# Kernel optimization log

Measured on AMD Instinct MI355X. Metric: run time of the kernel, lower is better.

Reference implementation:

```python
import jax, jax.numpy as jnp
import numpy as np

VOCAB = 100000
SHORTLIST = 10000  # cutoffs = [10000, 20000, 40000, 80000], n_clusters = 4
B, T, D = 1024, 128, 1024


def setup_inputs() -> dict:
    key = jax.random.key(0)
    ks = jax.random.split(key, 12)
    s = 0.02  # realistic init scale for weights
    inp = {
        "features": jax.random.normal(ks[0], (B, D), jnp.float32),
        "head_weight": jax.random.normal(ks[1], (SHORTLIST + 4, D), jnp.float32) * s,
        "proj0": jax.random.normal(ks[2], (512, D), jnp.float32) * s,
        "out0": jax.random.normal(ks[3], (10000, 512), jnp.float32) * s,
        "proj1": jax.random.normal(ks[4], (256, D), jnp.float32) * s,
        "out1": jax.random.normal(ks[5], (20000, 256), jnp.float32) * s,
        "proj2": jax.random.normal(ks[6], (128, D), jnp.float32) * s,
        "out2": jax.random.normal(ks[7], (40000, 128), jnp.float32) * s,
        "proj3": jax.random.normal(ks[8], (64, D), jnp.float32) * s,
        "out3": jax.random.normal(ks[9], (20000, 64), jnp.float32) * s,
        "discard_probs": jax.random.uniform(ks[10], (VOCAB,), jnp.float32),
        "targets": jax.random.randint(ks[11], (B, T), 0, VOCAB, jnp.int64),
        "target_mask": jnp.ones((B, T), jnp.bool_),
    }
    return inp


def _adaptive_log_prob(x, head_weight, projs, outs):
    # head: shortlist logits + one logit per tail cluster
    head_lp = jax.nn.log_softmax(x @ head_weight.T, axis=-1)  # [B, SHORTLIST+4]
    parts = [head_lp[:, :SHORTLIST]]
    for i, (pw, ow) in enumerate(zip(projs, outs)):
        cluster_logits = (x @ pw.T) @ ow.T  # [B, osz]
        parts.append(jax.nn.log_softmax(cluster_logits, axis=-1)
                     + head_lp[:, SHORTLIST + i:SHORTLIST + i + 1])
    return jnp.concatenate(parts, axis=-1)  # [B, VOCAB]


def reference(features, head_weight, proj0, out0, proj1, out1, proj2, out2,
              proj3, out3, discard_probs, targets, target_mask):
    # dropout is identity in eval/reference mode
    logprob = _adaptive_log_prob(features, head_weight,
                                 (proj0, proj1, proj2, proj3),
                                 (out0, out1, out2, out3))
    lp_t = jnp.take_along_axis(logprob, targets, axis=1)        # [B, T]
    w = (1.0 - discard_probs[targets]) * target_mask.astype(lp_t.dtype)
    per_sample = jnp.sum(-lp_t * w, axis=1) / jnp.sum(w, axis=1)  # [B]
    return jnp.sum(per_sample) / (targets.shape[0] + 1e-5)
```

## Files before the change

### kernel.cpp

```cpp
#include <hip/hip_runtime.h>
#include <cstdint>


typedef unsigned short u16;
typedef __attribute__((ext_vector_type(4))) float f32x4;
typedef __attribute__((ext_vector_type(8))) __bf16 bf16x8;
typedef __attribute__((ext_vector_type(4))) unsigned int u32x4;

__device__ __forceinline__ u16 f2bf(float f){
  unsigned u = __float_as_uint(f);
  u += 0x7FFFu + ((u >> 16) & 1u);
  return (u16)(u >> 16);
}

__device__ __forceinline__ float wave_sum(float v){
  #pragma unroll
  for (int d = 1; d < 64; d <<= 1) v += __shfl_xor(v, d, 64);
  return v;
}

__device__ __forceinline__ float wave_dot_l(const u16* a_lds, const u16* b, int len, int lane){
  float s = 0.f;
  for (int k = lane*8; k < len; k += 512){
    u32x4 va = *(const u32x4*)(a_lds + k);
    u32x4 vb = *(const u32x4*)(b + k);
    #pragma unroll
    for (int i = 0; i < 4; i++){
      unsigned ua = va[i], ub = vb[i];
      s = fmaf(__uint_as_float(ua << 16),        __uint_as_float(ub << 16),        s);
      s = fmaf(__uint_as_float(ua & 0xFFFF0000u), __uint_as_float(ub & 0xFFFF0000u), s);
    }
  }
  return wave_sum(s);
}

struct CvtSeg { const float* src; u16* dst; unsigned start; };
struct CvtTab { CvtSeg s[10]; unsigned total; };

__global__ __launch_bounds__(256) void cvt_bf16(CvtTab t){
  unsigned stride = gridDim.x * blockDim.x;
  for (unsigned c = blockIdx.x*blockDim.x + threadIdx.x; c < t.total; c += stride){
    int si = 0;
    #pragma unroll
    for (int i = 1; i < 10; i++) if (c >= t.s[i].start) si = i;
    unsigned lo = c - t.s[si].start;
    const float4* sp = (const float4*)t.s[si].src + (size_t)lo*2;
    float4 f0 = sp[0], f1 = sp[1];
    uint4 d;
    d.x = (unsigned)f2bf(f0.x) | ((unsigned)f2bf(f0.y) << 16);
    d.y = (unsigned)f2bf(f0.z) | ((unsigned)f2bf(f0.w) << 16);
    d.z = (unsigned)f2bf(f1.x) | ((unsigned)f2bf(f1.y) << 16);
    d.w = (unsigned)f2bf(f1.z) | ((unsigned)f2bf(f1.w) << 16);
    ((uint4*)t.s[si].dst)[lo] = d;
  }
}

struct GSeg { const u16* A; const u16* B; float* part; u16* C; float* gates;
              int lda, N, K, ntiles, tileStart, ldc; };
struct GTab { GSeg seg[5]; int nseg; };

__global__ __launch_bounds__(256, 3) void gemm_all(GTab tab){
  __shared__ u16 ldsA[128*64];
  __shared__ u16 ldsB[128*64];
  __shared__ float msLds[128][2];

  int by = blockIdx.y;
  int s = 0;
  #pragma unroll
  for (int i = 1; i < 5; i++)
    if (i < tab.nseg && by >= tab.seg[i].tileStart) s = i;
  const u16* Ab = tab.seg[s].A;
  const u16* Bb = tab.seg[s].B;
  float* part   = tab.seg[s].part;
  u16* Cc       = tab.seg[s].C;
  float* gatesp = tab.seg[s].gates;
  int lda = tab.seg[s].lda, N = tab.seg[s].N, K = tab.seg[s].K;
  int ntiles = tab.seg[s].ntiles, ldc = tab.seg[s].ldc;
  int tileN = by - tab.seg[s].tileStart;
  int n0 = tileN * 128;
  int row0 = blockIdx.x * 128;

  int tid = threadIdx.x;
  int wid = tid >> 6, lane = tid & 63;
  int wr = wid >> 1, wc = wid & 1;
  int qr = lane >> 4, ln = lane & 15;

  const char* baseA = (const char*)(Ab + (size_t)row0*lda);
  const char* baseB = (const char*)Bb;
  unsigned offA[4], offB[4];
  #pragma unroll
  for (int t = 0; t < 4; t++){
    int c = t*256 + tid, row = c >> 3, jj = (c & 7) ^ (row & 7);
    offA[t] = (unsigned)(row*lda + jj*8) * 2u;
    int nr = n0 + row; if (nr >= N) nr = N - 1;
    offB[t] = (unsigned)(nr*K + jj*8) * 2u;
  }

  u32x4 pa[4], pb[4];
  #pragma unroll
  for (int t = 0; t < 4; t++){ pa[t] = *(const u32x4*)(baseA + offA[t]);
                               pb[t] = *(const u32x4*)(baseB + offB[t]); }

  f32x4 acc[4][4];
  const f32x4 zero = {0.f, 0.f, 0.f, 0.f};
  #pragma unroll
  for (int i = 0; i < 4; i++)
    #pragma unroll
    for (int j = 0; j < 4; j++) acc[i][j] = zero;

  int nkt = K >> 6;
  for (int kt = 0; kt < nkt; kt++){
    __syncthreads();
    #pragma unroll
    for (int t = 0; t < 4; t++){
      *(u32x4*)((char*)ldsA + (size_t)(t*256 + tid)*16) = pa[t];
      *(u32x4*)((char*)ldsB + (size_t)(t*256 + tid)*16) = pb[t];
    }
    __syncthreads();
    if (kt + 1 < nkt){
      unsigned kb = (unsigned)(kt + 1) * 128u;
      #pragma unroll
      for (int t = 0; t < 4; t++){ pa[t] = *(const u32x4*)(baseA + offA[t] + kb);
                                   pb[t] = *(const u32x4*)(baseB + offB[t] + kb); }
    }
    #pragma unroll
    for (int ks = 0; ks < 2; ks++){
      bf16x8 av[4], bv[4];
      #pragma unroll
      for (int mt = 0; mt < 4; mt++){
        int rl = wr*64 + mt*16 + ln;
        int ch = rl*8 + ((ks*4 + qr) ^ (rl & 7));
        av[mt] = *(const bf16x8*)((const char*)ldsA + ch*16);
      }
      #pragma unroll
      for (int nt = 0; nt < 4; nt++){
        int rl = wc*64 + nt*16 + ln;
        int ch = rl*8 + ((ks*4 + qr) ^ (rl & 7));
        bv[nt] = *(const bf16x8*)((const char*)ldsB + ch*16);
      }
      #pragma unroll
      for (int mt = 0; mt < 4; mt++)
        #pragma unroll
        for (int nt = 0; nt < 4; nt++)
          acc[mt][nt] = __builtin_amdgcn_mfma_f32_16x16x32_bf16(av[mt], bv[nt], acc[mt][nt], 0, 0, 0);
    }
  }

  if (part){
    #pragma unroll
    for (int mt = 0; mt < 4; mt++){
      #pragma unroll
      for (int r = 0; r < 4; r++){
        float ss = 0.f;
        #pragma unroll
        for (int nt = 0; nt < 4; nt++){
          int col = n0 + wc*64 + nt*16 + ln;
          if (col < N){
            float v = acc[mt][nt][r];
            ss += __expf(v);
            if (gatesp && col >= 10000){
              int row = row0 + wr*64 + mt*16 + qr*4 + r;
              gatesp[row*4 + (col - 10000)] = v;
            }
          }
        }
        ss += __shfl_xor(ss, 1, 64);
        ss += __shfl_xor(ss, 2, 64);
        ss += __shfl_xor(ss, 4, 64);
        ss += __shfl_xor(ss, 8, 64);
        if (ln == 0) msLds[wr*64 + mt*16 + qr*4 + r][wc] = ss;
      }
    }
    __syncthreads();
    if (tid < 128)
      part[(size_t)(row0 + tid)*ntiles + tileN] = msLds[tid][0] + msLds[tid][1];
  } else {
    #pragma unroll
    for (int mt = 0; mt < 4; mt++)
      #pragma unroll
      for (int nt = 0; nt < 4; nt++)
        #pragma unroll
        for (int r = 0; r < 4; r++){
          int col = n0 + wc*64 + nt*16 + ln;
          if (col < N){
            int row = row0 + wr*64 + mt*16 + qr*4 + r;
            Cc[(size_t)row*ldc + col] = f2bf(acc[mt][nt][r]);
          }
        }
  }
}

struct LseTab { const float* base[5]; int ntiles[5]; float* lse; };

__global__ __launch_bounds__(256) void lse_reduce(LseTab t){
  int widx = blockIdx.x*4 + (threadIdx.x >> 6);
  int lane = threadIdx.x & 63;
  int mat = widx >> 10, row = widx & 1023;
  const float* p = t.base[mat] + (size_t)row * t.ntiles[mat];
  float s = 0.f;
  for (int i = lane; i < t.ntiles[mat]; i += 64) s += p[i];
  s = wave_sum(s);
  if (lane == 0) t.lse[mat*1024 + row] = __logf(s);
}

struct GatherArgs {
  const u16* Xb; const u16* Hb; const u16* Hact; const u16* Ob;
  const float* lse; const float* gates; const int* targets; float* lp;
};

__global__ __launch_bounds__(256) void gather_rows(GatherArgs g){
  __shared__ u16 xr[1024];
  __shared__ u16 hr[960];
  __shared__ int tg[128];
  __shared__ float ls[5], gs[4];

  int b = blockIdx.x;
  int tid = threadIdx.x;
  int w = tid >> 6, lane = tid & 63;

  if (tid < 128) ((u32x4*)xr)[tid] = ((const u32x4*)(g.Xb + (size_t)b*1024))[tid];
  else if (tid < 248) ((u32x4*)hr)[tid-128] = ((const u32x4*)(g.Hact + (size_t)b*960))[tid-128];
  if (tid < 32) ((u32x4*)tg)[tid] = ((const u32x4*)(g.targets + (size_t)b*128))[tid];
  if (tid < 5) ls[tid] = g.lse[tid*1024 + b];
  if (tid < 4) gs[tid] = g.gates[b*4 + tid];
  __syncthreads();

  for (int t = 0; t < 32; t++){
    int ti = w*32 + t;
    int v = tg[ti];
    float val;
    if (v < 10000){
      float logit = wave_dot_l(xr, g.Hb + (size_t)v*1024, 1024, lane);
      val = logit - ls[0];
    } else {
      int c, off, psz, hoff; size_t oboff;
      if      (v < 20000){ c=0; off=10000; psz=512; hoff=0;   oboff=0; }
      else if (v < 40000){ c=1; off=20000; psz=256; hoff=512; oboff=5120000; }
      else if (v < 80000){ c=2; off=40000; psz=128; hoff=768; oboff=10240000; }
      else               { c=3; off=80000; psz=64;  hoff=896; oboff=15360000; }
      float logit = wave_dot_l(hr + hoff, g.Ob + oboff + (size_t)(v - off)*psz, psz, lane);
      val = gs[c] - ls[0] + logit - ls[c + 1];
    }
    if (lane == 0) g.lp[b*128 + ti] = val;
  }
}

__global__ __launch_bounds__(128) void row_loss(const float* lp, const int* targets,
                                                const float* discard, float* psamp){
  int b = blockIdx.x, t = threadIdx.x;
  int idx = b*128 + t;
  int v = targets[idx];
  float w = 1.0f - discard[v];
  float a = -lp[idx] * w;
  float as = wave_sum(a), ws = wave_sum(w);
  __shared__ float sa[2], sw[2];
  int wid = t >> 6, lane = t & 63;
  if (lane == 0){ sa[wid] = as; sw[wid] = ws; }
  __syncthreads();
  if (t == 0) psamp[b] = (sa[0] + sa[1]) / (sw[0] + sw[1]);
}

__global__ __launch_bounds__(256) void final_sum(const float* psamp, float* out){
  float s = 0.f;
  for (int i = threadIdx.x; i < 1024; i += 256) s += psamp[i];
  s = wave_sum(s);
  __shared__ float sb[4];
  if ((threadIdx.x & 63) == 0) sb[threadIdx.x >> 6] = s;
  __syncthreads();
  if (threadIdx.x == 0) out[0] = (sb[0] + sb[1] + sb[2] + sb[3]) / (1024.0f + 1e-5f);
}

extern "C" void kernel_launch(void* const* d_in, const int* in_sizes, int n_in,
                              void* d_out, int out_size, void* d_ws, size_t ws_size,
                              hipStream_t stream){
  (void)in_sizes; (void)n_in; (void)out_size; (void)ws_size;
  const float* features = (const float*)d_in[0];
  const float* head_w   = (const float*)d_in[1];
  const float* proj[4]  = {(const float*)d_in[2], (const float*)d_in[4],
                           (const float*)d_in[6], (const float*)d_in[8]};
  const float* outw[4]  = {(const float*)d_in[3], (const float*)d_in[5],
                           (const float*)d_in[7], (const float*)d_in[9]};
  const float* discard  = (const float*)d_in[10];
  const int*   targets  = (const int*)d_in[11];
  float* out = (float*)d_out;

  char* wsp = (char*)d_ws;
  size_t off = 0;
  auto carve = [&](size_t bytes)->char*{
    char* p = wsp + off; off += (bytes + 255) & ~(size_t)255; return p;
  };
  u16* Xb     = (u16*)carve(1024ull*1024*2);
  u16* Hb     = (u16*)carve(10004ull*1024*2);
  u16* Pb     = (u16*)carve(960ull*1024*2);
  u16* Ob     = (u16*)carve(16640000ull*2);
  u16* Hact   = (u16*)carve(1024ull*960*2);
  float* part = (float*)carve(803840ull*4);
  float* lse  = (float*)carve(5*1024*4);
  float* gates= (float*)carve(4096*4);
  float* lp   = (float*)carve(131072ull*4);
  float* psamp= (float*)carve(1024*4);

  CvtTab ct{};
  const float* srcs[10] = {features, head_w, proj[0], proj[1], proj[2], proj[3],
                           outw[0], outw[1], outw[2], outw[3]};
  u16* dsts[10] = {Xb, Hb, Pb, Pb + 512*1024, Pb + 768*1024, Pb + 896*1024,
                   Ob, Ob + 5120000, Ob + 10240000, Ob + 15360000};
  unsigned counts[10] = {1048576u, 10244096u, 524288u, 262144u, 131072u, 65536u,
                         5120000u, 5120000u, 5120000u, 1280000u};
  unsigned pre = 0;
  for (int i = 0; i < 10; i++){
    ct.s[i].src = srcs[i]; ct.s[i].dst = dsts[i]; ct.s[i].start = pre;
    pre += counts[i] / 8;
  }
  ct.total = pre;
  cvt_bf16<<<dim3(4096), dim3(256), 0, stream>>>(ct);

  float* pHead = part;
  float* pC0 = part + 80896;
  float* pC1 = part + 161792;
  float* pC2 = part + 322560;
  float* pC3 = part + 643072;

  GTab tp{};
  tp.nseg = 4;
  tp.seg[0] = {Xb, Pb,            nullptr, Hact,       nullptr, 1024, 512, 1024, 4, 0, 960};
  tp.seg[1] = {Xb, Pb + 512*1024, nullptr, Hact + 512, nullptr, 1024, 256, 1024, 2, 4, 960};
  tp.seg[2] = {Xb, Pb + 768*1024, nullptr, Hact + 768, nullptr, 1024, 128, 1024, 1, 6, 960};
  tp.seg[3] = {Xb, Pb + 896*1024, nullptr, Hact + 896, nullptr, 1024, 64,  1024, 1, 7, 960};
  gemm_all<<<dim3(8, 8), dim3(256), 0, stream>>>(tp);

  GTab tm{};
  tm.nseg = 5;
  tm.seg[0] = {Xb,         Hb,            pHead, nullptr, gates,   1024, 10004, 1024, 79,  0,   0};
  tm.seg[1] = {Hact,       Ob,            pC0,   nullptr, nullptr, 960,  10000, 512,  79,  79,  0};
  tm.seg[2] = {Hact + 512, Ob + 5120000,  pC1,   nullptr, nullptr, 960,  20000, 256,  157, 158, 0};
  tm.seg[3] = {Hact + 768, Ob + 10240000, pC2,   nullptr, nullptr, 960,  40000, 128,  313, 315, 0};
  tm.seg[4] = {Hact + 896, Ob + 15360000, pC3,   nullptr, nullptr, 960,  20000, 64,   157, 628, 0};
  gemm_all<<<dim3(8, 785), dim3(256), 0, stream>>>(tm);

  LseTab lt{};
  lt.base[0] = pHead; lt.base[1] = pC0; lt.base[2] = pC1; lt.base[3] = pC2; lt.base[4] = pC3;
  lt.ntiles[0] = 79; lt.ntiles[1] = 79; lt.ntiles[2] = 157; lt.ntiles[3] = 313; lt.ntiles[4] = 157;
  lt.lse = lse;
  lse_reduce<<<dim3(1280), dim3(256), 0, stream>>>(lt);

  GatherArgs ga{Xb, Hb, Hact, Ob, lse, gates, targets, lp};
  gather_rows<<<dim3(1024), dim3(256), 0, stream>>>(ga);

  row_loss<<<dim3(1024), dim3(128), 0, stream>>>(lp, targets, discard, psamp);
  final_sum<<<dim3(1), dim3(256), 0, stream>>>(psamp, out);
}
```

Baseline: 316.5 us.

## Use direct global-to-LDS loads, XCD-aware tile swizzle, fuse row loss into gather

The GEMM kernel now loads tiles straight into LDS with global_load_lds instead of staging them through registers, and drops the register prefetch of the next k-tile. Occupancy hint rises from 3 to 4 blocks per CU. The large logits GEMM remaps block indices so neighbouring N tiles land on the same XCD for L2 reuse of the shared A rows. The per-row loss reduction is fused into gather_rows, removing one kernel launch and the lp round trip through global memory. The price is that loads are no longer overlapped with compute within a block, and the code relies on the LDS layout written by global_load_lds matching the old per-thread layout.

```diff
diff --git a/kernel.cpp b/kernel.cpp
--- a/kernel.cpp
+++ b/kernel.cpp
@@ -32,6 +32,12 @@
     }
   }
   return wave_sum(s);
+}
+
+__device__ __forceinline__ void gload_lds16(const void* g, void* l){
+  __builtin_amdgcn_global_load_lds(
+      (const __attribute__((address_space(1))) unsigned int*)g,
+      (__attribute__((address_space(3))) unsigned int*)l, 16, 0, 0);
 }
 
 struct CvtSeg { const float* src; u16* dst; unsigned start; };
@@ -57,14 +63,23 @@
 
 struct GSeg { const u16* A; const u16* B; float* part; u16* C; float* gates;
               int lda, N, K, ntiles, tileStart, ldc; };
-struct GTab { GSeg seg[5]; int nseg; };
-
-__global__ __launch_bounds__(256, 3) void gemm_all(GTab tab){
-  __shared__ u16 ldsA[128*64];
-  __shared__ u16 ldsB[128*64];
+struct GTab { GSeg seg[5]; int nseg; int swz; };
+
+__global__ __launch_bounds__(256, 4) void gemm_all(GTab tab){
+  __shared__ __attribute__((aligned(16))) u16 ldsA[128*64];
+  __shared__ __attribute__((aligned(16))) u16 ldsB[128*64];
   __shared__ float msLds[128][2];
 
-  int by = blockIdx.y;
+  int bx = blockIdx.x, by = blockIdx.y;
+  if (tab.swz){
+    int flat = by * 8 + bx;
+    int xcd = flat & 7, j = flat >> 3;
+    by = (j >> 3) * 8 + xcd;
+    bx = j & 7;
+    int nby = (int)gridDim.y;
+    if (by >= nby){ by = nby - 1; bx = xcd; }
+  }
+
   int s = 0;
   #pragma unroll
   for (int i = 1; i < 5; i++)
@@ -78,7 +93,7 @@
   int ntiles = tab.seg[s].ntiles, ldc = tab.seg[s].ldc;
   int tileN = by - tab.seg[s].tileStart;
   int n0 = tileN * 128;
-  int row0 = blockIdx.x * 128;
+  int row0 = bx * 128;
 
   int tid = threadIdx.x;
   int wid = tid >> 6, lane = tid & 63;
@@ -95,11 +110,7 @@
     int nr = n0 + row; if (nr >= N) nr = N - 1;
     offB[t] = (unsigned)(nr*K + jj*8) * 2u;
   }
-
-  u32x4 pa[4], pb[4];
-  #pragma unroll
-  for (int t = 0; t < 4; t++){ pa[t] = *(const u32x4*)(baseA + offA[t]);
-                               pb[t] = *(const u32x4*)(baseB + offB[t]); }
+  unsigned ldsWave = (unsigned)(wid << 6) * 16u;
 
   f32x4 acc[4][4];
   const f32x4 zero = {0.f, 0.f, 0.f, 0.f};
@@ -111,18 +122,13 @@
   int nkt = K >> 6;
   for (int kt = 0; kt < nkt; kt++){
     __syncthreads();
+    unsigned kb = (unsigned)kt * 128u;
     #pragma unroll
     for (int t = 0; t < 4; t++){
-      *(u32x4*)((char*)ldsA + (size_t)(t*256 + tid)*16) = pa[t];
-      *(u32x4*)((char*)ldsB + (size_t)(t*256 + tid)*16) = pb[t];
+      gload_lds16(baseA + offA[t] + kb, (char*)ldsA + (unsigned)t*4096u + ldsWave);
+      gload_lds16(baseB + offB[t] + kb, (char*)ldsB + (unsigned)t*4096u + ldsWave);
     }
     __syncthreads();
-    if (kt + 1 < nkt){
-      unsigned kb = (unsigned)(kt + 1) * 128u;
-      #pragma unroll
-      for (int t = 0; t < 4; t++){ pa[t] = *(const u32x4*)(baseA + offA[t] + kb);
-                                   pb[t] = *(const u32x4*)(baseB + offB[t] + kb); }
-    }
     #pragma unroll
     for (int ks = 0; ks < 2; ks++){
       bf16x8 av[4], bv[4];
@@ -205,14 +211,17 @@
 
 struct GatherArgs {
   const u16* Xb; const u16* Hb; const u16* Hact; const u16* Ob;
-  const float* lse; const float* gates; const int* targets; float* lp;
+  const float* lse; const float* gates; const int* targets;
+  const float* discard; float* psamp;
 };
 
 __global__ __launch_bounds__(256) void gather_rows(GatherArgs g){
-  __shared__ u16 xr[1024];
-  __shared__ u16 hr[960];
-  __shared__ int tg[128];
+  __shared__ __attribute__((aligned(16))) u16 xr[1024];
+  __shared__ __attribute__((aligned(16))) u16 hr[960];
+  __shared__ __attribute__((aligned(16))) int tg[128];
   __shared__ float ls[5], gs[4];
+  __shared__ float lpv[128];
+  __shared__ float sa[2], sw[2];
 
   int b = blockIdx.x;
   int tid = threadIdx.x;
@@ -241,23 +250,19 @@
       float logit = wave_dot_l(hr + hoff, g.Ob + oboff + (size_t)(v - off)*psz, psz, lane);
       val = gs[c] - ls[0] + logit - ls[c + 1];
     }
-    if (lane == 0) g.lp[b*128 + ti] = val;
-  }
-}
-
-__global__ __launch_bounds__(128) void row_loss(const float* lp, const int* targets,
-                                                const float* discard, float* psamp){
-  int b = blockIdx.x, t = threadIdx.x;
-  int idx = b*128 + t;
-  int v = targets[idx];
-  float w = 1.0f - discard[v];
-  float a = -lp[idx] * w;
-  float as = wave_sum(a), ws = wave_sum(w);
-  __shared__ float sa[2], sw[2];
-  int wid = t >> 6, lane = t & 63;
-  if (lane == 0){ sa[wid] = as; sw[wid] = ws; }
+    if (lane == 0) lpv[ti] = val;
+  }
   __syncthreads();
-  if (t == 0) psamp[b] = (sa[0] + sa[1]) / (sw[0] + sw[1]);
+
+  if (tid < 128){
+    int v = tg[tid];
+    float wt = 1.0f - g.discard[v];
+    float a  = -lpv[tid] * wt;
+    float as = wave_sum(a), ws = wave_sum(wt);
+    if (lane == 0){ sa[w] = as; sw[w] = ws; }
+  }
+  __syncthreads();
+  if (tid == 0) g.psamp[b] = (sa[0] + sa[1]) / (sw[0] + sw[1]);
 }
 
 __global__ __launch_bounds__(256) void final_sum(const float* psamp, float* out){
@@ -297,7 +302,6 @@
   float* part = (float*)carve(803840ull*4);
   float* lse  = (float*)carve(5*1024*4);
   float* gates= (float*)carve(4096*4);
-  float* lp   = (float*)carve(131072ull*4);
   float* psamp= (float*)carve(1024*4);
 
   CvtTab ct{};
@@ -322,7 +326,7 @@
   float* pC3 = part + 643072;
 
   GTab tp{};
-  tp.nseg = 4;
+  tp.nseg = 4; tp.swz = 0;
   tp.seg[0] = {Xb, Pb,            nullptr, Hact,       nullptr, 1024, 512, 1024, 4, 0, 960};
   tp.seg[1] = {Xb, Pb + 512*1024, nullptr, Hact + 512, nullptr, 1024, 256, 1024, 2, 4, 960};
   tp.seg[2] = {Xb, Pb + 768*1024, nullptr, Hact + 768, nullptr, 1024, 128, 1024, 1, 6, 960};
@@ -330,7 +334,7 @@
   gemm_all<<<dim3(8, 8), dim3(256), 0, stream>>>(tp);
 
   GTab tm{};
-  tm.nseg = 5;
+  tm.nseg = 5; tm.swz = 1;
   tm.seg[0] = {Xb,         Hb,            pHead, nullptr, gates,   1024, 10004, 1024, 79,  0,   0};
   tm.seg[1] = {Hact,       Ob,            pC0,   nullptr, nullptr, 960,  10000, 512,  79,  79,  0};
   tm.seg[2] = {Hact + 512, Ob + 5120000,  pC1,   nullptr, nullptr, 960,  20000, 256,  157, 158, 0};
@@ -344,9 +348,8 @@
   lt.lse = lse;
   lse_reduce<<<dim3(1280), dim3(256), 0, stream>>>(lt);
 
-  GatherArgs ga{Xb, Hb, Hact, Ob, lse, gates, targets, lp};
+  GatherArgs ga{Xb, Hb, Hact, Ob, lse, gates, targets, discard, psamp};
   gather_rows<<<dim3(1024), dim3(256), 0, stream>>>(ga);
 
-  row_loss<<<dim3(1024), dim3(128), 0, stream>>>(lp, targets, discard, psamp);
   final_sum<<<dim3(1), dim3(256), 0, stream>>>(psamp, out);
 }
```

New measurement: 297.0 us. 6.2% less time.
